# Performance work log

Measured on AMD Instinct MI355X. Metric: run time of the kernel, lower is better.

Reference implementation:

```python
import jax, jax.numpy as jnp
import numpy as np

B, S, D_IN = 2, 2048, 1024
EMBED, HEADS = 1024, 16
HEAD_DIM = EMBED // HEADS

def setup_inputs() -> dict:
    key = jax.random.key(0)
    k1, k2, k3 = jax.random.split(key, 3)
    # xavier_uniform bounds
    def xavier(k, shape):
        fan_in, fan_out = shape[1], shape[0]
        lim = jnp.sqrt(6.0 / (fan_in + fan_out))
        return jax.random.uniform(k, shape, jnp.float32, -lim, lim)
    x = jax.random.normal(k1, (B, S, D_IN), jnp.float32)
    qkv_w = xavier(k2, (3 * EMBED, D_IN))   # torch Linear weight layout [out, in]
    qkv_b = jnp.zeros((3 * EMBED,), jnp.float32)
    o_w = xavier(k3, (EMBED, EMBED))
    o_b = jnp.zeros((EMBED,), jnp.float32)
    return {"x": x, "qkv_w": qkv_w, "qkv_b": qkv_b, "o_w": o_w, "o_b": o_b}

def reference(x, qkv_w, qkv_b, o_w, o_b):
    Bq, Sq, _ = x.shape
    qkv = x @ qkv_w.T + qkv_b                       # [B,S,3E]
    qkv = qkv.reshape(Bq, Sq, HEADS, 3 * HEAD_DIM).transpose(0, 2, 1, 3)  # [B,H,S,3d]
    q, k, v = jnp.split(qkv, 3, axis=-1)            # each [B,H,S,d]
    scale = 1.0 / jnp.sqrt(jnp.asarray(HEAD_DIM, x.dtype))
    logits = jnp.einsum('bhqd,bhkd->bhqk', q, k) * scale
    attn = jax.nn.softmax(logits, axis=-1)
    vals = jnp.einsum('bhqk,bhkd->bhqd', attn, v)   # [B,H,S,d]
    vals = vals.transpose(0, 2, 1, 3).reshape(Bq, Sq, EMBED)
    return vals @ o_w.T + o_b
```

## Files before the change

kernel.cpp:

```cpp
#include <hip/hip_runtime.h>
#include <hip/hip_bf16.h>

#define B_    2
#define S_    2048
#define DIN   1024
#define EMB   1024
#define NH    16
#define HD    64
#define N3    3072
#define MROWS 4096
#define KVB   64
#define QBLK  128
#define NT    (S_ / KVB)

typedef short bf16x8 __attribute__((ext_vector_type(8)));
typedef float f32x4  __attribute__((ext_vector_type(4)));
typedef float f32x16 __attribute__((ext_vector_type(16)));
typedef unsigned short u16;
typedef u16 u16x8 __attribute__((ext_vector_type(8)));
typedef u16 u16x4 __attribute__((ext_vector_type(4)));
typedef unsigned int u32;

__device__ __forceinline__ u16 f2bf(float f) {
  union { float f; unsigned u; } x; x.f = f;
  unsigned r = x.u + 0x7fffu + ((x.u >> 16) & 1u);
  return (u16)(r >> 16);
}

__device__ __forceinline__ u32 cvtpk(float lo, float hi) {
  u32 r;
  asm("v_cvt_pk_bf16_f32 %0, %1, %2" : "=v"(r) : "v"(lo), "v"(hi));
  return r;
}

__device__ __forceinline__ void gload16(const void* g, void* l) {
  __builtin_amdgcn_global_load_lds(
      (const __attribute__((address_space(1))) unsigned int*)g,
      (__attribute__((address_space(3))) unsigned int*)l, 16, 0, 0);
}

__global__ void cast4(const float* __restrict__ in, u16* __restrict__ out, int n4) {
  const int i = blockIdx.x * 256 + threadIdx.x;
  if (i < n4) {
    const float4 v = ((const float4*)in)[i];
    u16x4 o;
    o[0] = f2bf(v.x); o[1] = f2bf(v.y); o[2] = f2bf(v.z); o[3] = f2bf(v.w);
    ((u16x4*)out)[i] = o;
  }
}

template<int EPI>
__global__ __launch_bounds__(256)
void gemm_bt(const u16* __restrict__ A, const u16* __restrict__ W,
             const float* __restrict__ bias, float* __restrict__ Cf,
             u16* __restrict__ Qb, u16* __restrict__ Kb, u16* __restrict__ VbT,
             int M, int N, int K) {
  __shared__ u16 Als[128 * 32];
  __shared__ u16 Bls[128 * 32];
  const int tid  = threadIdx.x;
  const int wave = tid >> 6, lane = tid & 63;
  const int lhi  = lane >> 4, llo = lane & 15;
  const int wr   = wave >> 1, wc = wave & 1;
  const int m0   = blockIdx.y * 128, n0 = blockIdx.x * 128;

  const f32x4 fzero = {0.f, 0.f, 0.f, 0.f};
  f32x4 acc[4][4];
#pragma unroll
  for (int m = 0; m < 4; ++m)
#pragma unroll
    for (int n = 0; n < 4; ++n) acc[m][n] = fzero;

  for (int k0 = 0; k0 < K; k0 += 32) {
#pragma unroll
    for (int i = 0; i < 2; ++i) {
      const int e   = (tid + i * 256) * 8;
      const int row = e >> 5, col = e & 31;
      gload16(A + (size_t)(m0 + row) * K + k0 + col, (char*)Als + wave * 1024 + i * 4096);
      gload16(W + (size_t)(n0 + row) * K + k0 + col, (char*)Bls + wave * 1024 + i * 4096);
    }
    __syncthreads();
    bf16x8 af[4], bfr[4];
#pragma unroll
    for (int m = 0; m < 4; ++m) af[m]  = *(const bf16x8*)&Als[(wr * 64 + m * 16 + llo) * 32 + lhi * 8];
#pragma unroll
    for (int n = 0; n < 4; ++n) bfr[n] = *(const bf16x8*)&Bls[(wc * 64 + n * 16 + llo) * 32 + lhi * 8];
#pragma unroll
    for (int m = 0; m < 4; ++m)
#pragma unroll
      for (int n = 0; n < 4; ++n)
        acc[m][n] = __builtin_amdgcn_mfma_f32_16x16x32_bf16(af[m], bfr[n], acc[m][n], 0, 0, 0);
    __syncthreads();
  }

#pragma unroll
  for (int n = 0; n < 4; ++n) {
    const int colb = n0 + wc * 64 + n * 16;
    const int gcol = colb + llo;
    const float bv = bias[gcol];
    if (EPI == 0) {
      const int h   = colb / 192;
      const int rr  = colb - h * 192;
      const int sec = rr >> 6;
      const int d   = (rr & 63) + llo;
#pragma unroll
      for (int m = 0; m < 4; ++m) {
        const int rowb = m0 + wr * 64 + m * 16 + lhi * 4;
        const int b = rowb >> 11, s0 = rowb & 2047;
        if (sec == 2) {
          u16x4 vv;
#pragma unroll
          for (int r = 0; r < 4; ++r) vv[r] = f2bf(acc[m][n][r] + bv);
          *(u16x4*)&VbT[((size_t)(b * NH + h) * HD + d) * S_ + s0] = vv;
        } else {
          u16* dst = (sec == 0) ? Qb : Kb;
          const float scl = (sec == 0) ? 0.18033688f : 1.0f;
#pragma unroll
          for (int r = 0; r < 4; ++r)
            dst[(((size_t)(b * NH + h) * S_ + s0 + r) << 6) + d] = f2bf((acc[m][n][r] + bv) * scl);
        }
      }
    } else {
#pragma unroll
      for (int m = 0; m < 4; ++m) {
        const int rowb = m0 + wr * 64 + m * 16 + lhi * 4;
#pragma unroll
        for (int r = 0; r < 4; ++r)
          Cf[(size_t)(rowb + r) * N + gcol] = acc[m][n][r] + bv;
      }
    }
  }
}

__global__ __launch_bounds__(256)
void attn_fwd(const u16* __restrict__ Qb, const u16* __restrict__ Kb,
              const u16* __restrict__ VbT, u16* __restrict__ Obf) {
  __shared__ __align__(16) u16 Kls[4][KVB * HD];
  __shared__ __align__(16) u16 Vls[4][HD * KVB];
  __shared__ __align__(16) float sBc[4][32];
  const int tid  = threadIdx.x;
  const int wave = tid >> 6, lane = tid & 63;
  const int q    = lane & 31, hi = lane >> 5;
  const int bh   = blockIdx.y;
  const int q0   = blockIdx.x * QBLK;
  const size_t base  = (size_t)bh * S_ * HD;
  const size_t basev = (size_t)bh * HD * S_;

  const int qrow = q0 + wave * 32 + q;
  bf16x8 qf[4];
#pragma unroll
  for (int c = 0; c < 4; ++c)
    qf[c] = *(const bf16x8*)&Qb[base + (size_t)qrow * HD + c * 16 + hi * 8];

  const int srow = tid >> 3;
  const int xs   = (tid & 7) ^ (srow & 7);
  const u16* kSrc = Kb  + base  + (size_t)srow * HD + xs * 8;
  const u16* vSrc = VbT + basev + (size_t)srow * S_ + xs * 8;
  const int ldsW = wave * 1024;

  const int gq = 16 * (q >> 4) + 8 * ((q >> 2) & 1) + (q & 3) + 4 * ((q >> 3) & 1);

  int offK[2][4], offV[2][4];
#pragma unroll
  for (int b = 0; b < 2; ++b)
#pragma unroll
    for (int c = 0; c < 4; ++c) {
      offK[b][c] = (b * 32 + gq) * 128 + (((c * 2 + hi) ^ (gq & 7)) << 4);
      offV[b][c] = (b * 32 + q)  * 128 + (((c * 2 + hi) ^ (q  & 7)) << 4);
    }

  f32x16 o0, o1;
#pragma unroll
  for (int r = 0; r < 16; ++r) { o0[r] = 0.f; o1[r] = 0.f; }
  float m_run = -1e30f, lsum = 0.f;

  auto issue = [&](int t) {
#pragma unroll
    for (int p = 0; p < 2; ++p) {
      gload16(kSrc + (size_t)t * KVB * HD + (size_t)p * 32 * HD,
              (char*)Kls[t & 3] + p * 4096 + ldsW);
      gload16(vSrc + t * KVB + (size_t)p * 32 * S_,
              (char*)Vls[t & 3] + p * 4096 + ldsW);
    }
  };

  auto compute = [&](int t) {
    const char* Kt = (const char*)Kls[t & 3];
    const char* Vt = (const char*)Vls[t & 3];

    f32x16 s0, s1;
#pragma unroll
    for (int r = 0; r < 16; ++r) { s0[r] = 0.f; s1[r] = 0.f; }
    __builtin_amdgcn_s_setprio(1);
#pragma unroll
    for (int c = 0; c < 4; ++c) {
      bf16x8 k0 = *(const bf16x8*)(Kt + offK[0][c]);
      bf16x8 k1 = *(const bf16x8*)(Kt + offK[1][c]);
      s0 = __builtin_amdgcn_mfma_f32_32x32x16_bf16(k0, qf[c], s0, 0, 0, 0);
      s1 = __builtin_amdgcn_mfma_f32_32x32x16_bf16(k1, qf[c], s1, 0, 0, 0);
    }
    __builtin_amdgcn_s_setprio(0);

    float pm = fmaxf(s0[0], s1[0]);
#pragma unroll
    for (int r = 1; r < 16; ++r) pm = fmaxf(pm, fmaxf(s0[r], s1[r]));
    pm = fmaxf(pm, __shfl_xor(pm, 32));

    const float mnew  = fmaxf(m_run, pm);
    const float alpha = exp2f(m_run - mnew);

    sBc[wave][q] = alpha;
    asm volatile("s_waitcnt lgkmcnt(0)" ::: "memory");
    f32x4 av[4];
#pragma unroll
    for (int g = 0; g < 4; ++g) av[g] = *(const f32x4*)&sBc[wave][hi * 4 + g * 8];
#pragma unroll
    for (int r = 0; r < 16; ++r) {
      const float f = av[r >> 2][r & 3];
      o0[r] *= f; o1[r] *= f;
    }

    float ts = 0.f;
    u32 dw0[8], dw1[8];
#pragma unroll
    for (int j = 0; j < 8; ++j) {
      const float a0 = exp2f(s0[2 * j] - mnew), a1 = exp2f(s0[2 * j + 1] - mnew);
      const float b0 = exp2f(s1[2 * j] - mnew), b1 = exp2f(s1[2 * j + 1] - mnew);
      ts += (a0 + a1) + (b0 + b1);
      dw0[j] = cvtpk(a0, a1);
      dw1[j] = cvtpk(b0, b1);
    }
    ts += __shfl_xor(ts, 32);
    lsum = lsum * alpha + ts;
    m_run = mnew;

    __builtin_amdgcn_s_setprio(1);
#pragma unroll
    for (int c = 0; c < 4; ++c) {
      union { u32 u[4]; bf16x8 v; } P;
      if (c == 0)      { P.u[0] = dw0[0]; P.u[1] = dw0[1]; P.u[2] = dw0[2]; P.u[3] = dw0[3]; }
      else if (c == 1) { P.u[0] = dw0[4]; P.u[1] = dw0[5]; P.u[2] = dw0[6]; P.u[3] = dw0[7]; }
      else if (c == 2) { P.u[0] = dw1[0]; P.u[1] = dw1[1]; P.u[2] = dw1[2]; P.u[3] = dw1[3]; }
      else             { P.u[0] = dw1[4]; P.u[1] = dw1[5]; P.u[2] = dw1[6]; P.u[3] = dw1[7]; }
      bf16x8 v0 = *(const bf16x8*)(Vt + offV[0][c]);
      bf16x8 v1 = *(const bf16x8*)(Vt + offV[1][c]);
      o0 = __builtin_amdgcn_mfma_f32_32x32x16_bf16(P.v, v0, o0, 0, 0, 0);
      o1 = __builtin_amdgcn_mfma_f32_32x32x16_bf16(P.v, v1, o1, 0, 0, 0);
    }
    __builtin_amdgcn_s_setprio(0);
  };

  issue(0); issue(1); issue(2);

#define BAR() do { asm volatile("" ::: "memory"); \
                   __builtin_amdgcn_s_barrier();  \
                   asm volatile("" ::: "memory"); } while (0)
  for (int t = 0; t < NT - 3; ++t) {
    issue(t + 3);
    asm volatile("s_waitcnt vmcnt(12)" ::: "memory");
    BAR();
    compute(t);
    BAR();
  }
  asm volatile("s_waitcnt vmcnt(8)" ::: "memory");
  BAR(); compute(NT - 3); BAR();
  asm volatile("s_waitcnt vmcnt(4)" ::: "memory");
  BAR(); compute(NT - 2); BAR();
  asm volatile("s_waitcnt vmcnt(0)" ::: "memory");
  BAR(); compute(NT - 1);
#undef BAR

  const float li = 1.0f / lsum;
  sBc[wave][q] = li;
  asm volatile("s_waitcnt lgkmcnt(0)" ::: "memory");
  f32x4 lv[4];
#pragma unroll
  for (int g = 0; g < 4; ++g) lv[g] = *(const f32x4*)&sBc[wave][hi * 4 + g * 8];
  const int b = bh >> 4, h = bh & 15;
#pragma unroll
  for (int r = 0; r < 16; ++r) {
    const int qg = q0 + wave * 32 + (r & 3) + 8 * (r >> 2) + 4 * hi;
    const float f = lv[r >> 2][r & 3];
    u16* dst = Obf + ((size_t)(b * S_ + qg) * NH + h) * HD;
    dst[q]      = f2bf(o0[r] * f);
    dst[32 + q] = f2bf(o1[r] * f);
  }
}

extern "C" void kernel_launch(void* const* d_in, const int* in_sizes, int n_in,
                              void* d_out, int out_size, void* d_ws, size_t ws_size,
                              hipStream_t stream) {
  const float* x     = (const float*)d_in[0];
  const float* qkv_w = (const float*)d_in[1];
  const float* qkv_b = (const float*)d_in[2];
  const float* o_w   = (const float*)d_in[3];
  const float* o_b   = (const float*)d_in[4];
  float* out = (float*)d_out;

  char* ws = (char*)d_ws;
  u16* xbf  = (u16*)(ws);
  u16* wqkv = (u16*)(ws + (8u  << 20));
  u16* wo   = (u16*)(ws + (14u << 20));
  u16* Qb   = (u16*)(ws + (16u << 20));
  u16* Kb   = (u16*)(ws + (24u << 20));
  u16* VbT  = (u16*)(ws + (32u << 20));
  u16* atnb = xbf;

  cast4<<<4096, 256, 0, stream>>>(x,     xbf,  1048576);
  cast4<<<3072, 256, 0, stream>>>(qkv_w, wqkv,  786432);
  cast4<<<1024, 256, 0, stream>>>(o_w,   wo,    262144);

  gemm_bt<0><<<dim3(N3 / 128, MROWS / 128), 256, 0, stream>>>(
      xbf, wqkv, qkv_b, nullptr, Qb, Kb, VbT, MROWS, N3, DIN);

  attn_fwd<<<dim3(S_ / QBLK, B_ * NH), 256, 0, stream>>>(Qb, Kb, VbT, atnb);

  gemm_bt<1><<<dim3(EMB / 128, MROWS / 128), 256, 0, stream>>>(
      atnb, wo, o_b, out, nullptr, nullptr, nullptr, MROWS, EMB, EMB);
}
```

Baseline: 161.1 us.

## Add lazy softmax rescaling and process KV tiles in pairs per barrier

Skips the running-max update and output rescale unless some lane's new max exceeds the stored max by more than a threshold, which removes the LDS broadcast and 32 multiplies in most iterations. The max reduction becomes a tree and the row-sum accumulation is split into independent partial sums for more ILP. The KV loop now issues two tiles at a time and computes two tiles between barriers, halving barrier count but using a different prefetch depth. Lazy rescaling lets exponentials grow up to 2^10 relative to the stored max, which keeps fp32 sums and bf16 P values in range but slightly changes rounding behaviour.

```diff
diff --git a/kernel.cpp b/kernel.cpp
--- a/kernel.cpp
+++ b/kernel.cpp
@@ -200,38 +200,45 @@
     }
     __builtin_amdgcn_s_setprio(0);
 
-    float pm = fmaxf(s0[0], s1[0]);
-#pragma unroll
-    for (int r = 1; r < 16; ++r) pm = fmaxf(pm, fmaxf(s0[r], s1[r]));
-    pm = fmaxf(pm, __shfl_xor(pm, 32));
-
-    const float mnew  = fmaxf(m_run, pm);
-    const float alpha = exp2f(m_run - mnew);
-
-    sBc[wave][q] = alpha;
-    asm volatile("s_waitcnt lgkmcnt(0)" ::: "memory");
-    f32x4 av[4];
-#pragma unroll
-    for (int g = 0; g < 4; ++g) av[g] = *(const f32x4*)&sBc[wave][hi * 4 + g * 8];
-#pragma unroll
-    for (int r = 0; r < 16; ++r) {
-      const float f = av[r >> 2][r & 3];
-      o0[r] *= f; o1[r] *= f;
-    }
-
-    float ts = 0.f;
+    float tm[16];
+#pragma unroll
+    for (int r = 0; r < 16; ++r) tm[r] = fmaxf(s0[r], s1[r]);
+#pragma unroll
+    for (int st = 8; st >= 1; st >>= 1)
+#pragma unroll
+      for (int i = 0; i < 16; ++i) if (i < st) tm[i] = fmaxf(tm[i], tm[i + st]);
+    const float pm = fmaxf(tm[0], __shfl_xor(tm[0], 32));
+
+    if (__any(pm > m_run + 10.0f)) {
+      const float mnew  = fmaxf(m_run, pm);
+      const float alpha = exp2f(m_run - mnew);
+      sBc[wave][q] = alpha;
+      asm volatile("s_waitcnt lgkmcnt(0)" ::: "memory");
+      f32x4 av[4];
+#pragma unroll
+      for (int g = 0; g < 4; ++g) av[g] = *(const f32x4*)&sBc[wave][hi * 4 + g * 8];
+#pragma unroll
+      for (int r = 0; r < 16; ++r) {
+        const float f = av[r >> 2][r & 3];
+        o0[r] *= f; o1[r] *= f;
+      }
+      lsum *= alpha;
+      m_run = mnew;
+    }
+
+    float t0 = 0.f, t1 = 0.f, t2 = 0.f, t3 = 0.f;
     u32 dw0[8], dw1[8];
 #pragma unroll
     for (int j = 0; j < 8; ++j) {
-      const float a0 = exp2f(s0[2 * j] - mnew), a1 = exp2f(s0[2 * j + 1] - mnew);
-      const float b0 = exp2f(s1[2 * j] - mnew), b1 = exp2f(s1[2 * j + 1] - mnew);
-      ts += (a0 + a1) + (b0 + b1);
+      const float a0 = exp2f(s0[2 * j] - m_run), a1 = exp2f(s0[2 * j + 1] - m_run);
+      const float b0 = exp2f(s1[2 * j] - m_run), b1 = exp2f(s1[2 * j + 1] - m_run);
+      t0 += a0; t1 += a1; t2 += b0; t3 += b1;
       dw0[j] = cvtpk(a0, a1);
       dw1[j] = cvtpk(b0, b1);
     }
+    float ts = (t0 + t1) + (t2 + t3);
     ts += __shfl_xor(ts, 32);
-    lsum = lsum * alpha + ts;
-    m_run = mnew;
+    lsum += ts;
 
     __builtin_amdgcn_s_setprio(1);
 #pragma unroll
@@ -249,24 +256,23 @@
     __builtin_amdgcn_s_setprio(0);
   };
 
-  issue(0); issue(1); issue(2);
+  issue(0); issue(1);
 
 #define BAR() do { asm volatile("" ::: "memory"); \
                    __builtin_amdgcn_s_barrier();  \
                    asm volatile("" ::: "memory"); } while (0)
-  for (int t = 0; t < NT - 3; ++t) {
-    issue(t + 3);
-    asm volatile("s_waitcnt vmcnt(12)" ::: "memory");
+  for (int p = 0; p < NT / 2 - 1; ++p) {
+    issue(2 * p + 2); issue(2 * p + 3);
+    asm volatile("s_waitcnt vmcnt(8)" ::: "memory");
     BAR();
-    compute(t);
+    compute(2 * p);
+    compute(2 * p + 1);
     BAR();
   }
-  asm volatile("s_waitcnt vmcnt(8)" ::: "memory");
-  BAR(); compute(NT - 3); BAR();
-  asm volatile("s_waitcnt vmcnt(4)" ::: "memory");
-  BAR(); compute(NT - 2); BAR();
   asm volatile("s_waitcnt vmcnt(0)" ::: "memory");
-  BAR(); compute(NT - 1);
+  BAR();
+  compute(NT - 2);
+  compute(NT - 1);
 #undef BAR
 
   const float li = 1.0f / lsum;
```

Measured after the change: 151.7 us. -5.8%, faster.
